# Performance work log

Hardware: AMD Instinct MI355X
Metric: run time of the kernel (lower is better)

Reference implementation:

```python
import jax, jax.numpy as jnp
import numpy as np

B, T, D_IN, H, D_OUT = 4096, 512, 8, 50, 1

def setup_inputs() -> dict:
    key = jax.random.key(0)
    ks = jax.random.split(key, 7)
    s_ih = 1.0 / np.sqrt(H)
    return {
        "x": jax.random.normal(ks[0], (B, T, D_IN), dtype=jnp.float32),
        # torch nn.RNN params: weight_ih_l0 [H, D_IN], weight_hh_l0 [H, H], biases [H]
        "W_ih": jax.random.uniform(ks[1], (H, D_IN), minval=-s_ih, maxval=s_ih, dtype=jnp.float32),
        "W_hh": jax.random.uniform(ks[2], (H, H), minval=-s_ih, maxval=s_ih, dtype=jnp.float32),
        "b_ih": jax.random.uniform(ks[3], (H,), minval=-s_ih, maxval=s_ih, dtype=jnp.float32),
        "b_hh": jax.random.uniform(ks[4], (H,), minval=-s_ih, maxval=s_ih, dtype=jnp.float32),
        # fc: Linear(H, D_OUT)
        "fc_W": jax.random.uniform(ks[5], (D_OUT, H), minval=-s_ih, maxval=s_ih, dtype=jnp.float32),
        "fc_b": jax.random.uniform(ks[6], (D_OUT,), minval=-s_ih, maxval=s_ih, dtype=jnp.float32),
    }

def reference(x, W_ih, W_hh, b_ih, b_hh, fc_W, fc_b):
    # Vanilla RNN: h_t = tanh(x_t @ W_ih^T + b_ih + h_{t-1} @ W_hh^T + b_hh)
    # Precompute input projections for all timesteps (one big GEMM),
    # then scan the recurrence over time. Only the last hidden state is
    # needed because the module reads out[:, -1, :].
    xW = jnp.einsum('btd,hd->bth', x, W_ih) + (b_ih + b_hh)  # [B, T, H]
    xW_t = jnp.swapaxes(xW, 0, 1)  # [T, B, H] for scan over time

    def step(h, xw_t):
        h_new = jnp.tanh(xw_t + h @ W_hh.T)
        return h_new, None

    h0 = jnp.zeros((x.shape[0], W_hh.shape[0]), dtype=x.dtype)
    h_last, _ = jax.lax.scan(step, h0, xW_t)
    # fc on last timestep hidden
    return h_last @ fc_W.T + fc_b  # [B, D_OUT]
```

## Files before the change

kernel.cpp:

```cpp
#include <hip/hip_runtime.h>

#define B_TOT 4096
#define T_LEN 512
#define DIN   8
#define H_DIM 50

typedef __attribute__((ext_vector_type(8))) short  short8;
typedef __attribute__((ext_vector_type(4))) float  floatx4;

__device__ __forceinline__ ushort f2bf_rne(float f) {
  uint u = __float_as_uint(f);
  u += 0x7FFFu + ((u >> 16) & 1u);
  return (ushort)(u >> 16);
}
__device__ __forceinline__ ushort f2bf_trunc(float f) {
  return (ushort)(__float_as_uint(f) >> 16);
}
__device__ __forceinline__ float bf2f(ushort b) {
  return __uint_as_float(((uint)b) << 16);
}
__device__ __forceinline__ float fast_tanh(float v) {
  float e = __expf(2.0f * v);
  return 1.0f - 2.0f * __builtin_amdgcn_rcpf(1.0f + e);
}

#define ROWS 72
#define REG  1152

__global__ __launch_bounds__(256) void rnn_fused(
    const float* __restrict__ x, const float* __restrict__ W_ih,
    const float* __restrict__ W_hh, const float* __restrict__ b_ih,
    const float* __restrict__ b_hh, const float* __restrict__ fc_W,
    const float* __restrict__ fc_b, float* __restrict__ out)
{
  __shared__ __align__(16) ushort lds[4 * REG];

  const int tid  = threadIdx.x;
  const int lane = tid & 63;
  const int wave = tid >> 6;
  const int col  = lane & 15;
  const int kg   = lane >> 4;
  const int b0   = blockIdx.x * 16;

  const int iGlob = wave * 16 + col;
  union U8 { ushort u[8]; short8 v; };
  U8 Bh0u, Bh1u, Bl0u, Bl1u;
#pragma unroll
  for (int hf = 0; hf < 2; ++hf) {
#pragma unroll
    for (int j = 0; j < 8; ++j) {
      int k = hf * 32 + kg * 8 + j;
      float w = 0.f;
      if (iGlob < H_DIM) {
        if (k < H_DIM)            w = W_hh[iGlob * H_DIM + k];
        else if (k < H_DIM + DIN) w = W_ih[iGlob * DIN + (k - H_DIM)];
      }
      ushort hi = f2bf_rne(w);
      ushort lo = f2bf_trunc(w - bf2f(hi));
      if (hf == 0) { Bh0u.u[j] = hi; Bl0u.u[j] = lo; }
      else         { Bh1u.u[j] = hi; Bl1u.u[j] = lo; }
    }
  }
  const short8 Bh0 = Bh0u.v, Bh1 = Bh1u.v, Bl0 = Bl0u.v, Bl1 = Bl1u.v;

  const float bv = (iGlob < H_DIM) ? (b_ih[iGlob] + b_hh[iGlob]) : 0.f;
  const floatx4 biasf = {bv, bv, bv, bv};

  for (int z = tid; z < 4 * REG; z += 256) lds[z] = 0;
  __syncthreads();

  const int xm = tid >> 3;
  const int xd = tid & 7;
  const float* xp = x + ((size_t)(b0 + ((tid < 128) ? xm : 0)) * T_LEN) * DIN + xd;
  float px1 = 0.f, px2 = 0.f, px3 = 0.f;
  if (tid < 128) {
    float x0 = xp[0];
    ushort xh = f2bf_rne(x0);
    lds[0 * REG + xm * ROWS + H_DIM + xd] = xh;
    lds[1 * REG + xm * ROWS + H_DIM + xd] = f2bf_trunc(x0 - bf2f(xh));
    px1 = xp[8]; px2 = xp[16]; px3 = xp[24];
  }
  __syncthreads();

  auto step = [&](int t, int offph, int offpl, int offqh, int offql) {
    const int rb = col * ROWS + kg * 8;
    short8 Ah0 = *(const short8*)(lds + offph + rb);
    short8 Ah1 = *(const short8*)(lds + offph + rb + 32);
    short8 Al0 = *(const short8*)(lds + offpl + rb);
    short8 Al1 = *(const short8*)(lds + offpl + rb + 32);

    floatx4 acc = biasf;
    acc = __builtin_amdgcn_mfma_f32_16x16x32_bf16(Ah0, Bh0, acc, 0, 0, 0);
    acc = __builtin_amdgcn_mfma_f32_16x16x32_bf16(Ah1, Bh1, acc, 0, 0, 0);
    acc = __builtin_amdgcn_mfma_f32_16x16x32_bf16(Al0, Bh0, acc, 0, 0, 0);
    acc = __builtin_amdgcn_mfma_f32_16x16x32_bf16(Al1, Bh1, acc, 0, 0, 0);
    floatx4 accB = {0.f, 0.f, 0.f, 0.f};
    accB = __builtin_amdgcn_mfma_f32_16x16x32_bf16(Ah0, Bl0, accB, 0, 0, 0);
    accB = __builtin_amdgcn_mfma_f32_16x16x32_bf16(Ah1, Bl1, accB, 0, 0, 0);

    if (iGlob < H_DIM) {
#pragma unroll
      for (int r = 0; r < 4; ++r) {
        float v  = acc[r] + accB[r];
        float th = fast_tanh(v);
        ushort hi = f2bf_rne(th);
        ushort lo = f2bf_trunc(th - bf2f(hi));
        int m = kg * 4 + r;
        lds[offqh + m * ROWS + iGlob] = hi;
        lds[offql + m * ROWS + iGlob] = lo;
      }
    }
    if (tid < 128) {
      ushort xh = f2bf_rne(px1);
      ushort xl = f2bf_trunc(px1 - bf2f(xh));
      lds[offqh + xm * ROWS + H_DIM + xd] = xh;
      lds[offql + xm * ROWS + H_DIM + xd] = xl;
      px1 = px2; px2 = px3;
      int tn = t + 4; if (tn > T_LEN - 1) tn = T_LEN - 1;
      px3 = xp[tn * 8];
    }
    __syncthreads();
  };

  for (int t = 0; t < T_LEN; t += 2) {
    step(t,     0 * REG, 1 * REG, 2 * REG, 3 * REG);
    step(t + 1, 2 * REG, 3 * REG, 0 * REG, 1 * REG);
  }

  if (tid < 64) {
    int m = tid >> 2, kq = tid & 3;
    float acc2 = 0.f;
    for (int k = kq; k < H_DIM; k += 4) {
      float hv = bf2f(lds[0 * REG + m * ROWS + k]) + bf2f(lds[1 * REG + m * ROWS + k]);
      acc2 += hv * fc_W[k];
    }
    acc2 += __shfl_xor(acc2, 1);
    acc2 += __shfl_xor(acc2, 2);
    if (kq == 0) out[b0 + m] = acc2 + fc_b[0];
  }
}

extern "C" void kernel_launch(void* const* d_in, const int* in_sizes, int n_in,
                              void* d_out, int out_size, void* d_ws, size_t ws_size,
                              hipStream_t stream) {
  const float* x    = (const float*)d_in[0];
  const float* W_ih = (const float*)d_in[1];
  const float* W_hh = (const float*)d_in[2];
  const float* b_ih = (const float*)d_in[3];
  const float* b_hh = (const float*)d_in[4];
  const float* fc_W = (const float*)d_in[5];
  const float* fc_b = (const float*)d_in[6];
  rnn_fused<<<dim3(B_TOT / 16), dim3(256), 0, stream>>>(
      x, W_ih, W_hh, b_ih, b_hh, fc_W, fc_b, (float*)d_out);
}
```

Measured before the change: 294.8 us.

## Halve batch rows per block to double grid parallelism across CUs

Each block now handles 8 batch rows instead of 16, doubling the number of blocks to spread the sequential recurrence over more CUs. The x prefetch moves to wave 3, and the epilogue runs only on lanes holding valid rows. The hi/lo bf16 split now uses truncation instead of round-to-nearest. The six MFMAs are regrouped into three independent accumulator chains to shorten the dependency chain. Half of each MFMA tile's rows are now padding, so matrix work per useful row doubles.

```diff
diff --git a/kernel.cpp b/kernel.cpp
--- a/kernel.cpp
+++ b/kernel.cpp
@@ -4,6 +4,7 @@
 #define T_LEN 512
 #define DIN   8
 #define H_DIM 50
+#define BPB   8
 
 typedef __attribute__((ext_vector_type(8))) short  short8;
 typedef __attribute__((ext_vector_type(4))) float  floatx4;
@@ -40,7 +41,7 @@
   const int wave = tid >> 6;
   const int col  = lane & 15;
   const int kg   = lane >> 4;
-  const int b0   = blockIdx.x * 16;
+  const int b0   = blockIdx.x * BPB;
 
   const int iGlob = wave * 16 + col;
   union U8 { ushort u[8]; short8 v; };
@@ -69,18 +70,20 @@
   for (int z = tid; z < 4 * REG; z += 256) lds[z] = 0;
   __syncthreads();
 
-  const int xm = tid >> 3;
-  const int xd = tid & 7;
-  const float* xp = x + ((size_t)(b0 + ((tid < 128) ? xm : 0)) * T_LEN) * DIN + xd;
+  const int xm = lane >> 3;
+  const int xd = lane & 7;
+  const float* xp = x + ((size_t)(b0 + xm) * T_LEN) * DIN + xd;
   float px1 = 0.f, px2 = 0.f, px3 = 0.f;
-  if (tid < 128) {
+  if (wave == 3) {
     float x0 = xp[0];
-    ushort xh = f2bf_rne(x0);
+    ushort xh = f2bf_trunc(x0);
     lds[0 * REG + xm * ROWS + H_DIM + xd] = xh;
     lds[1 * REG + xm * ROWS + H_DIM + xd] = f2bf_trunc(x0 - bf2f(xh));
     px1 = xp[8]; px2 = xp[16]; px3 = xp[24];
   }
   __syncthreads();
+
+  const bool epi = (iGlob < H_DIM) && (kg < 2);
 
   auto step = [&](int t, int offph, int offpl, int offqh, int offql) {
     const int rb = col * ROWS + kg * 8;
@@ -89,35 +92,37 @@
     short8 Al0 = *(const short8*)(lds + offpl + rb);
     short8 Al1 = *(const short8*)(lds + offpl + rb + 32);
 
-    floatx4 acc = biasf;
-    acc = __builtin_amdgcn_mfma_f32_16x16x32_bf16(Ah0, Bh0, acc, 0, 0, 0);
-    acc = __builtin_amdgcn_mfma_f32_16x16x32_bf16(Ah1, Bh1, acc, 0, 0, 0);
-    acc = __builtin_amdgcn_mfma_f32_16x16x32_bf16(Al0, Bh0, acc, 0, 0, 0);
-    acc = __builtin_amdgcn_mfma_f32_16x16x32_bf16(Al1, Bh1, acc, 0, 0, 0);
+    floatx4 accA = biasf;
+    accA = __builtin_amdgcn_mfma_f32_16x16x32_bf16(Ah0, Bh0, accA, 0, 0, 0);
+    accA = __builtin_amdgcn_mfma_f32_16x16x32_bf16(Ah1, Bh1, accA, 0, 0, 0);
     floatx4 accB = {0.f, 0.f, 0.f, 0.f};
     accB = __builtin_amdgcn_mfma_f32_16x16x32_bf16(Ah0, Bl0, accB, 0, 0, 0);
     accB = __builtin_amdgcn_mfma_f32_16x16x32_bf16(Ah1, Bl1, accB, 0, 0, 0);
+    floatx4 accC = {0.f, 0.f, 0.f, 0.f};
+    accC = __builtin_amdgcn_mfma_f32_16x16x32_bf16(Al0, Bh0, accC, 0, 0, 0);
+    accC = __builtin_amdgcn_mfma_f32_16x16x32_bf16(Al1, Bh1, accC, 0, 0, 0);
 
-    if (iGlob < H_DIM) {
+    if (epi) {
 #pragma unroll
       for (int r = 0; r < 4; ++r) {
-        float v  = acc[r] + accB[r];
+        float v  = accA[r] + accB[r] + accC[r];
         float th = fast_tanh(v);
-        ushort hi = f2bf_rne(th);
-        ushort lo = f2bf_trunc(th - bf2f(hi));
+        uint  u  = __float_as_uint(th);
+        float hf2 = __uint_as_float(u & 0xFFFF0000u);
+        float lf  = th - hf2;
         int m = kg * 4 + r;
-        lds[offqh + m * ROWS + iGlob] = hi;
-        lds[offql + m * ROWS + iGlob] = lo;
+        lds[offqh + m * ROWS + iGlob] = (ushort)(u >> 16);
+        lds[offql + m * ROWS + iGlob] = f2bf_trunc(lf);
       }
     }
-    if (tid < 128) {
-      ushort xh = f2bf_rne(px1);
+    if (wave == 3) {
+      ushort xh = f2bf_trunc(px1);
       ushort xl = f2bf_trunc(px1 - bf2f(xh));
       lds[offqh + xm * ROWS + H_DIM + xd] = xh;
       lds[offql + xm * ROWS + H_DIM + xd] = xl;
       px1 = px2; px2 = px3;
       int tn = t + 4; if (tn > T_LEN - 1) tn = T_LEN - 1;
-      px3 = xp[tn * 8];
+      px3 = xp[tn * DIN];
     }
     __syncthreads();
   };
@@ -127,7 +132,7 @@
     step(t + 1, 2 * REG, 3 * REG, 0 * REG, 1 * REG);
   }
 
-  if (tid < 64) {
+  if (tid < BPB * 4) {
     int m = tid >> 2, kq = tid & 3;
     float acc2 = 0.f;
     for (int k = kq; k < H_DIM; k += 4) {
@@ -150,6 +155,6 @@
   const float* b_hh = (const float*)d_in[4];
   const float* fc_W = (const float*)d_in[5];
   const float* fc_b = (const float*)d_in[6];
-  rnn_fused<<<dim3(B_TOT / 16), dim3(256), 0, stream>>>(
+  rnn_fused<<<dim3(B_TOT / BPB), dim3(256), 0, stream>>>(
       x, W_ih, W_hh, b_ih, b_hh, fc_W, fc_b, (float*)d_out);
 }
```

New measurement: 321.0 us. +8.9%, slower.
